# Kernel optimization log

Hardware: AMD Instinct MI355X
Metric: run time of the kernel (lower is better)

The kernel has to match this reference:

```python
import jax, jax.numpy as jnp
import numpy as np

N_ITER = 5
NMF_EPS = 1e-20
IP_EPS = 1e-20

M, J, I, K = 2, 2000, 2049, 8  # channels == sources, frames, freq bins, NMF bases


def setup_inputs() -> dict:
    key = jax.random.key(0)
    k1, k2, k3 = jax.random.split(key, 3)
    X = jax.random.normal(k1, (M, J, I, 2), dtype=jnp.float32)
    lo = 1e-08
    T0 = jax.random.uniform(k2, (I, K, M), dtype=jnp.float32) * (1 - lo) + lo
    V0 = jax.random.uniform(k3, (K, J, M), dtype=jnp.float32) * (1 - lo) + lo
    return {"X": X, "T0": T0, "V0": V0}


def nmf_update(T, V, Y, eps):
    # T: (I,K), V: (K,J), Y: (I,J) complex
    P = jnp.abs(Y) ** 2                       # power spectrogram (I,J)
    R = T @ V                                  # low-rank model (I,J)
    T = T * jnp.sqrt(((P / (R * R)) @ V.T) / ((1.0 / R) @ V.T))
    T = jnp.maximum(T, eps)
    R = T @ V
    V = V * jnp.sqrt((T.T @ (P / (R * R))) / (T.T @ (1.0 / R)))
    V = jnp.maximum(V, eps)
    R = T @ V
    return T, V, R


def reference(X, T0, V0):
    Mc, Jc, Ic, _ = X.shape
    N = Mc
    # view_as_complex(X.permute(2,0,1,3)) -> (I, M, J) complex
    Xc = jnp.transpose(X[..., 0] + 1j * X[..., 1], (2, 0, 1)).astype(jnp.complex64)
    eye_M = jnp.eye(Mc, dtype=jnp.complex64)
    W = jnp.broadcast_to(eye_M, (Ic, N, Mc))   # (I, N, M)
    T, V = T0, V0

    def body(carry, _):
        W, T, V = carry
        Y = jnp.einsum('inm,imj->inj', W, Xc)  # (I, N, J)
        for n in range(N):
            Tn, Vn, Rn = nmf_update(T[:, :, n], V[:, :, n], Y[:, n, :], NMF_EPS)
            T = T.at[:, :, n].set(Tn)
            V = V.at[:, :, n].set(Vn)
            inv_Rn = 1.0 / (Rn + IP_EPS)                       # (I, J)
            Xw = Xc * jnp.sqrt(inv_Rn)[:, None, :]             # (I, M, J)
            D = jnp.einsum('imj,ikj->imk', Xw, jnp.conj(Xw)) / Jc  # (I, M, M)
            Dreg = D + IP_EPS * eye_M
            A = jnp.einsum('inm,imk->ink', W, Dreg)            # (I, M, M)
            e_n = jnp.broadcast_to(eye_M[:, n], (Ic, Mc))
            b = jnp.linalg.solve(A, e_n[..., None])[..., 0]    # (I, M)
            quad = jnp.einsum('im,imk,ik->i', jnp.conj(b), Dreg, b)
            denom = jnp.sqrt(jnp.real(quad) + IP_EPS)          # (I,)
            W = W.at[:, n, :].set(jnp.conj(b / denom[:, None]))
        return (W, T, V), None

    (W, T, V), _ = jax.lax.scan(body, (W, T, V), None, length=N_ITER)
    Y = jnp.einsum('inm,imj->inj', W, Xc)                      # (I, N, J)
    Yp = jnp.transpose(Y, (1, 2, 0))                           # (N, J, I)
    return jnp.stack([jnp.real(Yp), jnp.imag(Yp)], axis=-1)    # (N, J, I, 2)
```

## Files before the change

### kernel.cpp

```cpp
#include <hip/hip_runtime.h>
#include <hip/hip_bf16.h>

#define M_CH 2
#define J_F 2000
#define I_F 2049
#define K_B 8
#define N_IT 5
#define NMF_EPS 1e-20f
#define IP_EPS 1e-20f

__global__ void k_init(const float* __restrict__ T0, const float* __restrict__ V0,
                       float* __restrict__ T, float* __restrict__ V, float* __restrict__ W) {
  int t = blockIdx.x * blockDim.x + threadIdx.x;
  int stride = gridDim.x * blockDim.x;
  for (int idx = t; idx < 2 * I_F * K_B; idx += stride) {
    int n = idx / (I_F * K_B);
    int r = idx % (I_F * K_B);
    int i = r / K_B, k = r % K_B;
    T[idx] = T0[(i * K_B + k) * M_CH + n];
  }
  for (int idx = t; idx < 2 * K_B * J_F; idx += stride) {
    int n = idx / (K_B * J_F);
    int r = idx % (K_B * J_F);
    int k = r / J_F, j = r % J_F;
    V[idx] = V0[(k * J_F + j) * M_CH + n];
  }
  for (int i = t; i < I_F; i += stride) {
    W[i * 8 + 0] = 1.f; W[i * 8 + 1] = 0.f; W[i * 8 + 2] = 0.f; W[i * 8 + 3] = 0.f;
    W[i * 8 + 4] = 0.f; W[i * 8 + 5] = 0.f; W[i * 8 + 6] = 1.f; W[i * 8 + 7] = 0.f;
  }
}

__global__ __launch_bounds__(256) void k_pack(const float2* __restrict__ X,
                                              float4* __restrict__ Xp) {
  const int i = blockIdx.x * 256 + threadIdx.x;
  if (i >= I_F) return;
  const int j0 = blockIdx.y * 8;
  const int jend = min(8, J_F - j0);
  for (int jj = 0; jj < jend; ++jj) {
    const int j = j0 + jj;
    float2 a = X[(size_t)j * I_F + i];
    float2 b = X[(size_t)(J_F + j) * I_F + i];
    Xp[(size_t)j * I_F + i] = make_float4(a.x, a.y, b.x, b.y);
  }
}

__global__ __launch_bounds__(256) void k_packT(const float2* __restrict__ X,
                                               float4* __restrict__ Xpt) {
  __shared__ float4 Tl[32][33];
  const int tid = threadIdx.x;
  const int i0 = blockIdx.x * 32, j0 = blockIdx.y * 32;
  const int la = tid & 31, su = tid >> 5;
#pragma unroll
  for (int p = 0; p < 4; ++p) {
    int jj = su + p * 8;
    int i = i0 + la, j = j0 + jj;
    if (i < I_F && j < J_F) {
      float2 a = X[(size_t)j * I_F + i];
      float2 b = X[(size_t)(J_F + j) * I_F + i];
      Tl[la][jj] = make_float4(a.x, a.y, b.x, b.y);
    }
  }
  __syncthreads();
#pragma unroll
  for (int p = 0; p < 4; ++p) {
    int ii = su + p * 8;
    int i = i0 + ii, j = j0 + la;
    if (i < I_F && j < J_F) Xpt[(size_t)i * J_F + j] = Tl[ii][la];
  }
}

__device__ __forceinline__ float4 load_x(const float4* Xp, const float2* X,
                                         int pk, size_t j, int i) {
  if (pk) return Xp[j * I_F + i];
  float2 a = X[j * I_F + i];
  float2 b = X[(size_t)J_F * I_F + j * I_F + i];
  return make_float4(a.x, a.y, b.x, b.y);
}

__device__ __forceinline__ float4 load_xt(const float4* Xpt, const float2* X,
                                          int pk, int i, int j) {
  if (pk) return Xpt[(size_t)i * J_F + j];
  float2 a = X[(size_t)j * I_F + i];
  float2 b = X[(size_t)(J_F + j) * I_F + i];
  return make_float4(a.x, a.y, b.x, b.y);
}

template<int PK>
__global__ __launch_bounds__(256) void k_T_rows(const float4* __restrict__ Xpt,
                                                const float2* __restrict__ X,
                                                const float* __restrict__ W,
                                                float* __restrict__ T,
                                                const float* __restrict__ V) {
  const int i = blockIdx.x;
  const int tid = threadIdx.x;
  float tr0[K_B], tr1[K_B];
#pragma unroll
  for (int k = 0; k < K_B; ++k) {
    tr0[k] = T[(size_t)i * 8 + k];
    tr1[k] = T[((size_t)I_F + i) * 8 + k];
  }
  const float4 w0 = ((const float4*)W)[i * 2];
  const float4 w1 = ((const float4*)W)[i * 2 + 1];
  float num0[K_B] = {}, den0[K_B] = {}, num1[K_B] = {}, den1[K_B] = {};
  for (int j = tid; j < J_F; j += 256) {
    float4 x = load_xt(Xpt, X, PK, i, j);
    float yr = w0.x * x.x - w0.y * x.y + w0.z * x.z - w0.w * x.w;
    float yi = w0.x * x.y + w0.y * x.x + w0.z * x.w + w0.w * x.z;
    float p0 = yr * yr + yi * yi;
    float zr = w1.x * x.x - w1.y * x.y + w1.z * x.z - w1.w * x.w;
    float zi = w1.x * x.y + w1.y * x.x + w1.z * x.w + w1.w * x.z;
    float p1 = zr * zr + zi * zi;
    float v0[K_B], v1[K_B];
    float R0 = 0.f, R1 = 0.f;
#pragma unroll
    for (int k = 0; k < K_B; ++k) {
      v0[k] = V[(size_t)k * J_F + j];           R0 += tr0[k] * v0[k];
      v1[k] = V[(size_t)(K_B + k) * J_F + j];   R1 += tr1[k] * v1[k];
    }
    float a0 = p0 / (R0 * R0), b0 = 1.0f / R0;
    float a1 = p1 / (R1 * R1), b1 = 1.0f / R1;
#pragma unroll
    for (int k = 0; k < K_B; ++k) {
      num0[k] += a0 * v0[k]; den0[k] += b0 * v0[k];
      num1[k] += a1 * v1[k]; den1[k] += b1 * v1[k];
    }
  }
  __shared__ float red[4][32];
  const int lane = tid & 63, wid = tid >> 6;
#pragma unroll
  for (int k = 0; k < K_B; ++k) {
    float a0 = num0[k], b0 = den0[k], a1 = num1[k], b1 = den1[k];
#pragma unroll
    for (int off = 32; off > 0; off >>= 1) {
      a0 += __shfl_xor(a0, off, 64);
      b0 += __shfl_xor(b0, off, 64);
      a1 += __shfl_xor(a1, off, 64);
      b1 += __shfl_xor(b1, off, 64);
    }
    if (lane == 0) {
      red[wid][k] = a0; red[wid][8 + k] = b0;
      red[wid][16 + k] = a1; red[wid][24 + k] = b1;
    }
  }
  __syncthreads();
  if (tid < 32) red[0][tid] = red[0][tid] + red[1][tid] + red[2][tid] + red[3][tid];
  __syncthreads();
  if (tid < 16) {
    int n = tid >> 3, k = tid & 7;
    float nu = red[0][n * 16 + k];
    float de = red[0][n * 16 + 8 + k];
    size_t idx = ((size_t)n * I_F + i) * 8 + k;
    float told = T[idx];
    T[idx] = fmaxf(told * sqrtf(nu / de), NMF_EPS);
  }
}

template<int PK>
__global__ __launch_bounds__(256) void k_v_update(const float4* __restrict__ Xp,
                                                  const float2* __restrict__ X,
                                                  const float* __restrict__ W,
                                                  const float* __restrict__ T,
                                                  float* __restrict__ V) {
  const int j = blockIdx.x;
  const int tid = threadIdx.x;
  float vold0[K_B], vold1[K_B];
#pragma unroll
  for (int k = 0; k < K_B; ++k) {
    vold0[k] = V[(size_t)k * J_F + j];
    vold1[k] = V[(size_t)(K_B + k) * J_F + j];
  }
  float num0[K_B] = {}, den0[K_B] = {}, num1[K_B] = {}, den1[K_B] = {};
  const float* T1 = T + (size_t)I_F * K_B;
  for (int i = tid; i < I_F; i += 256) {
    float4 x = load_x(Xp, X, PK, (size_t)j, i);
    const float4 wa = ((const float4*)W)[i * 2];
    const float4 wb = ((const float4*)W)[i * 2 + 1];
    float yr = wa.x * x.x - wa.y * x.y + wa.z * x.z - wa.w * x.w;
    float yi = wa.x * x.y + wa.y * x.x + wa.z * x.w + wa.w * x.z;
    float p0 = yr * yr + yi * yi;
    float zr = wb.x * x.x - wb.y * x.y + wb.z * x.z - wb.w * x.w;
    float zi = wb.x * x.y + wb.y * x.x + wb.z * x.w + wb.w * x.z;
    float p1 = zr * zr + zi * zi;
    const float4 ta = *(const float4*)&T[i * 8];
    const float4 tb = *(const float4*)&T[i * 8 + 4];
    const float4 tc = *(const float4*)&T1[i * 8];
    const float4 td = *(const float4*)&T1[i * 8 + 4];
    float t0[K_B] = {ta.x, ta.y, ta.z, ta.w, tb.x, tb.y, tb.z, tb.w};
    float t1[K_B] = {tc.x, tc.y, tc.z, tc.w, td.x, td.y, td.z, td.w};
    float R0 = 0.f, R1 = 0.f;
#pragma unroll
    for (int k = 0; k < K_B; ++k) { R0 += t0[k] * vold0[k]; R1 += t1[k] * vold1[k]; }
    float a0 = p0 / (R0 * R0), b0 = 1.0f / R0;
    float a1 = p1 / (R1 * R1), b1 = 1.0f / R1;
#pragma unroll
    for (int k = 0; k < K_B; ++k) {
      num0[k] += a0 * t0[k]; den0[k] += b0 * t0[k];
      num1[k] += a1 * t1[k]; den1[k] += b1 * t1[k];
    }
  }
  __shared__ float red[4][32];
  const int lane = tid & 63, wid = tid >> 6;
#pragma unroll
  for (int k = 0; k < K_B; ++k) {
    float a0 = num0[k], b0 = den0[k], a1 = num1[k], b1 = den1[k];
#pragma unroll
    for (int off = 32; off > 0; off >>= 1) {
      a0 += __shfl_xor(a0, off, 64);
      b0 += __shfl_xor(b0, off, 64);
      a1 += __shfl_xor(a1, off, 64);
      b1 += __shfl_xor(b1, off, 64);
    }
    if (lane == 0) {
      red[wid][k] = a0; red[wid][8 + k] = b0;
      red[wid][16 + k] = a1; red[wid][24 + k] = b1;
    }
  }
  __syncthreads();
  if (tid < 32) red[0][tid] = red[0][tid] + red[1][tid] + red[2][tid] + red[3][tid];
  __syncthreads();
  if (tid < 16) {
    int n = tid >> 3, k = tid & 7;
    float nu = red[0][n * 16 + k];
    float de = red[0][n * 16 + 8 + k];
    size_t idx = ((size_t)n * K_B + k) * J_F + j;
    float vo = V[idx];
    V[idx] = fmaxf(vo * sqrtf(nu / de), NMF_EPS);
  }
}

template<int PK>
__global__ __launch_bounds__(256) void k_d_rows(const float4* __restrict__ Xpt,
                                                const float2* __restrict__ X,
                                                const float* __restrict__ T,
                                                const float* __restrict__ V,
                                                float* __restrict__ W) {
  const int i = blockIdx.x;
  const int tid = threadIdx.x;
  float tr0[K_B], tr1[K_B];
#pragma unroll
  for (int k = 0; k < K_B; ++k) {
    tr0[k] = T[(size_t)i * K_B + k];
    tr1[k] = T[((size_t)I_F + i) * K_B + k];
  }
  float acc[8] = {};
  for (int j = tid; j < J_F; j += 256) {
    float4 x = load_xt(Xpt, X, PK, i, j);
    float R0 = 0.f, R1 = 0.f;
#pragma unroll
    for (int k = 0; k < K_B; ++k) {
      R0 += tr0[k] * V[(size_t)k * J_F + j];
      R1 += tr1[k] * V[(size_t)(K_B + k) * J_F + j];
    }
    float wv0 = 1.0f / (R0 + IP_EPS);
    float wv1 = 1.0f / (R1 + IP_EPS);
    float p00 = x.x * x.x + x.y * x.y;
    float p11 = x.z * x.z + x.w * x.w;
    float pr = x.x * x.z + x.y * x.w;
    float pi = x.y * x.z - x.x * x.w;
    acc[0] += wv0 * p00; acc[1] += wv0 * p11; acc[2] += wv0 * pr; acc[3] += wv0 * pi;
    acc[4] += wv1 * p00; acc[5] += wv1 * p11; acc[6] += wv1 * pr; acc[7] += wv1 * pi;
  }
  __shared__ float red[4][8];
  const int lane = tid & 63, wid = tid >> 6;
#pragma unroll
  for (int v = 0; v < 8; ++v) {
    float a = acc[v];
#pragma unroll
    for (int off = 32; off > 0; off >>= 1) a += __shfl_xor(a, off, 64);
    if (lane == 0) red[wid][v] = a;
  }
  __syncthreads();
  if (tid < 8) red[0][tid] = red[0][tid] + red[1][tid] + red[2][tid] + red[3][tid];
  __syncthreads();
  if (tid == 0) {
    float4 wa = ((const float4*)W)[i * 2];
    float4 wb = ((const float4*)W)[i * 2 + 1];
    float w00r = wa.x, w00i = wa.y, w01r = wa.z, w01i = wa.w;
    float w10r = wb.x, w10i = wb.y, w11r = wb.z, w11i = wb.w;
    const float invJ = 1.0f / (float)J_F;
#pragma unroll
    for (int n = 0; n < 2; ++n) {
      float d00 = red[0][n * 4 + 0] * invJ + IP_EPS;
      float d11 = red[0][n * 4 + 1] * invJ + IP_EPS;
      float d01r = red[0][n * 4 + 2] * invJ;
      float d01i = red[0][n * 4 + 3] * invJ;
      float A00r = w00r * d00 + (w01r * d01r + w01i * d01i);
      float A00i = w00i * d00 + (w01i * d01r - w01r * d01i);
      float A01r = (w00r * d01r - w00i * d01i) + w01r * d11;
      float A01i = (w00r * d01i + w00i * d01r) + w01i * d11;
      float A10r = w10r * d00 + (w11r * d01r + w11i * d01i);
      float A10i = w10i * d00 + (w11i * d01r - w11r * d01i);
      float A11r = (w10r * d01r - w10i * d01i) + w11r * d11;
      float A11i = (w10r * d01i + w10i * d01r) + w11i * d11;
      float detr = (A00r * A11r - A00i * A11i) - (A01r * A10r - A01i * A10i);
      float deti = (A00r * A11i + A00i * A11r) - (A01r * A10i + A01i * A10r);
      float idet = 1.0f / (detr * detr + deti * deti);
      float n0r, n0i, n1r, n1i;
      if (n == 0) { n0r = A11r; n0i = A11i; n1r = -A10r; n1i = -A10i; }
      else        { n0r = -A01r; n0i = -A01i; n1r = A00r; n1i = A00i; }
      float b0r = (n0r * detr + n0i * deti) * idet;
      float b0i = (n0i * detr - n0r * deti) * idet;
      float b1r = (n1r * detr + n1i * deti) * idet;
      float b1i = (n1i * detr - n1r * deti) * idet;
      float cr = d01r * b1r - d01i * b1i;
      float ci = d01r * b1i + d01i * b1r;
      float quad = d00 * (b0r * b0r + b0i * b0i) + d11 * (b1r * b1r + b1i * b1i)
                 + 2.0f * (b0r * cr + b0i * ci);
      float s = 1.0f / sqrtf(quad + IP_EPS);
      if (n == 0) { w00r = b0r * s; w00i = -b0i * s; w01r = b1r * s; w01i = -b1i * s; }
      else        { w10r = b0r * s; w10i = -b0i * s; w11r = b1r * s; w11i = -b1i * s; }
    }
    ((float4*)W)[i * 2]     = make_float4(w00r, w00i, w01r, w01i);
    ((float4*)W)[i * 2 + 1] = make_float4(w10r, w10i, w11r, w11i);
  }
}

template<int PK>
__global__ __launch_bounds__(256) void k_final(const float4* __restrict__ Xp,
                                               const float2* __restrict__ X,
                                               const float* __restrict__ W,
                                               float2* __restrict__ out) {
  const int i = blockIdx.x * 256 + threadIdx.x;
  if (i >= I_F) return;
  const float4 wa = ((const float4*)W)[i * 2];
  const float4 wb = ((const float4*)W)[i * 2 + 1];
  const int j0 = blockIdx.y * 8;
  const int jend = min(8, J_F - j0);
  for (int jj = 0; jj < jend; ++jj) {
    const int j = j0 + jj;
    float4 x = load_x(Xp, X, PK, (size_t)j, i);
    float y0r = wa.x * x.x - wa.y * x.y + wa.z * x.z - wa.w * x.w;
    float y0i = wa.x * x.y + wa.y * x.x + wa.z * x.w + wa.w * x.z;
    out[(size_t)j * I_F + i] = make_float2(y0r, y0i);
    float y1r = wb.x * x.x - wb.y * x.y + wb.z * x.z - wb.w * x.w;
    float y1i = wb.x * x.y + wb.y * x.x + wb.z * x.w + wb.w * x.z;
    out[(size_t)(J_F + j) * I_F + i] = make_float2(y1r, y1i);
  }
}

extern "C" void kernel_launch(void* const* d_in, const int* in_sizes, int n_in,
                              void* d_out, int out_size, void* d_ws, size_t ws_size,
                              hipStream_t stream) {
  const float2* X = (const float2*)d_in[0];
  const float* T0 = (const float*)d_in[1];
  const float* V0 = (const float*)d_in[2];
  char* ws = (char*)d_ws;
  size_t off = 0;
  auto alloc = [&](size_t bytes) -> void* {
    void* p = ws + off;
    off = (off + bytes + 255) & ~(size_t)255;
    return p;
  };
  float* W = (float*)alloc((size_t)I_F * 8 * 4);
  float* T = (float*)alloc((size_t)2 * I_F * K_B * 4);
  float* V = (float*)alloc((size_t)2 * K_B * J_F * 4);
  const size_t x_sz = (size_t)J_F * I_F * 16;
  float4* Xpt = nullptr;
  float4* Xp = nullptr;
  if (off + x_sz <= ws_size) Xpt = (float4*)alloc(x_sz);
  if (Xpt && off + x_sz <= ws_size) Xp = (float4*)alloc(x_sz);
  const int pkt = Xpt != nullptr, pkj = Xp != nullptr;

  k_init<<<128, 256, 0, stream>>>(T0, V0, T, V, W);
  if (pkt) k_packT<<<dim3(65, 63), 256, 0, stream>>>(X, Xpt);
  if (pkj) k_pack<<<dim3(9, 250), 256, 0, stream>>>(X, Xp);

  if (pkt && pkj) {
    for (int it = 0; it < N_IT; ++it) {
      k_T_rows<1><<<I_F, 256, 0, stream>>>(Xpt, X, W, T, V);
      k_v_update<1><<<J_F, 256, 0, stream>>>(Xp, X, W, T, V);
      k_d_rows<1><<<I_F, 256, 0, stream>>>(Xpt, X, T, V, W);
    }
    k_final<1><<<dim3(9, 250), 256, 0, stream>>>(Xp, X, W, (float2*)d_out);
  } else if (pkt) {
    for (int it = 0; it < N_IT; ++it) {
      k_T_rows<1><<<I_F, 256, 0, stream>>>(Xpt, X, W, T, V);
      k_v_update<0><<<J_F, 256, 0, stream>>>(nullptr, X, W, T, V);
      k_d_rows<1><<<I_F, 256, 0, stream>>>(Xpt, X, T, V, W);
    }
    k_final<0><<<dim3(9, 250), 256, 0, stream>>>(nullptr, X, W, (float2*)d_out);
  } else {
    for (int it = 0; it < N_IT; ++it) {
      k_T_rows<0><<<I_F, 256, 0, stream>>>(nullptr, X, W, T, V);
      k_v_update<0><<<J_F, 256, 0, stream>>>(nullptr, X, W, T, V);
      k_d_rows<0><<<I_F, 256, 0, stream>>>(nullptr, X, T, V, W);
    }
    k_final<0><<<dim3(9, 250), 256, 0, stream>>>(nullptr, X, W, (float2*)d_out);
  }
}
```

Measured before the change: 490.2 us.

## Fuse D/W update with next-iteration T update and interleave T/V per row

```diff
diff --git a/kernel.cpp b/kernel.cpp
--- a/kernel.cpp
+++ b/kernel.cpp
@@ -1,5 +1,4 @@
 #include <hip/hip_runtime.h>
-#include <hip/hip_bf16.h>
 
 #define M_CH 2
 #define J_F 2000
@@ -9,66 +8,9 @@
 #define NMF_EPS 1e-20f
 #define IP_EPS 1e-20f
 
-__global__ void k_init(const float* __restrict__ T0, const float* __restrict__ V0,
-                       float* __restrict__ T, float* __restrict__ V, float* __restrict__ W) {
-  int t = blockIdx.x * blockDim.x + threadIdx.x;
-  int stride = gridDim.x * blockDim.x;
-  for (int idx = t; idx < 2 * I_F * K_B; idx += stride) {
-    int n = idx / (I_F * K_B);
-    int r = idx % (I_F * K_B);
-    int i = r / K_B, k = r % K_B;
-    T[idx] = T0[(i * K_B + k) * M_CH + n];
-  }
-  for (int idx = t; idx < 2 * K_B * J_F; idx += stride) {
-    int n = idx / (K_B * J_F);
-    int r = idx % (K_B * J_F);
-    int k = r / J_F, j = r % J_F;
-    V[idx] = V0[(k * J_F + j) * M_CH + n];
-  }
-  for (int i = t; i < I_F; i += stride) {
-    W[i * 8 + 0] = 1.f; W[i * 8 + 1] = 0.f; W[i * 8 + 2] = 0.f; W[i * 8 + 3] = 0.f;
-    W[i * 8 + 4] = 0.f; W[i * 8 + 5] = 0.f; W[i * 8 + 6] = 1.f; W[i * 8 + 7] = 0.f;
-  }
-}
-
-__global__ __launch_bounds__(256) void k_pack(const float2* __restrict__ X,
-                                              float4* __restrict__ Xp) {
-  const int i = blockIdx.x * 256 + threadIdx.x;
-  if (i >= I_F) return;
-  const int j0 = blockIdx.y * 8;
-  const int jend = min(8, J_F - j0);
-  for (int jj = 0; jj < jend; ++jj) {
-    const int j = j0 + jj;
-    float2 a = X[(size_t)j * I_F + i];
-    float2 b = X[(size_t)(J_F + j) * I_F + i];
-    Xp[(size_t)j * I_F + i] = make_float4(a.x, a.y, b.x, b.y);
-  }
-}
-
-__global__ __launch_bounds__(256) void k_packT(const float2* __restrict__ X,
-                                               float4* __restrict__ Xpt) {
-  __shared__ float4 Tl[32][33];
-  const int tid = threadIdx.x;
-  const int i0 = blockIdx.x * 32, j0 = blockIdx.y * 32;
-  const int la = tid & 31, su = tid >> 5;
-#pragma unroll
-  for (int p = 0; p < 4; ++p) {
-    int jj = su + p * 8;
-    int i = i0 + la, j = j0 + jj;
-    if (i < I_F && j < J_F) {
-      float2 a = X[(size_t)j * I_F + i];
-      float2 b = X[(size_t)(J_F + j) * I_F + i];
-      Tl[la][jj] = make_float4(a.x, a.y, b.x, b.y);
-    }
-  }
-  __syncthreads();
-#pragma unroll
-  for (int p = 0; p < 4; ++p) {
-    int ii = su + p * 8;
-    int i = i0 + ii, j = j0 + la;
-    if (i < I_F && j < J_F) Xpt[(size_t)i * J_F + j] = Tl[ii][la];
-  }
-}
+#define NB_PACKT (65 * 63)
+#define NB_PACK (9 * 250)
+#define NB_INIT 128
 
 __device__ __forceinline__ float4 load_x(const float4* Xp, const float2* X,
                                          int pk, size_t j, int i) {
@@ -86,38 +28,101 @@
   return make_float4(a.x, a.y, b.x, b.y);
 }
 
-template<int PK>
-__global__ __launch_bounds__(256) void k_T_rows(const float4* __restrict__ Xpt,
-                                                const float2* __restrict__ X,
-                                                const float* __restrict__ W,
-                                                float* __restrict__ T,
-                                                const float* __restrict__ V) {
-  const int i = blockIdx.x;
+template<int PKT, int PKJ>
+__global__ __launch_bounds__(256) void k_setup(const float2* __restrict__ X,
+                                               const float* __restrict__ T0,
+                                               const float* __restrict__ V0,
+                                               float* __restrict__ Tt,
+                                               float* __restrict__ Vt,
+                                               float* __restrict__ W,
+                                               float4* __restrict__ Xpt,
+                                               float4* __restrict__ Xp) {
+  int b = blockIdx.x;
   const int tid = threadIdx.x;
-  float tr0[K_B], tr1[K_B];
-#pragma unroll
-  for (int k = 0; k < K_B; ++k) {
-    tr0[k] = T[(size_t)i * 8 + k];
-    tr1[k] = T[((size_t)I_F + i) * 8 + k];
-  }
-  const float4 w0 = ((const float4*)W)[i * 2];
-  const float4 w1 = ((const float4*)W)[i * 2 + 1];
+  if (b < NB_PACKT) {
+    if (!PKT) return;
+    __shared__ float4 Tl[32][33];
+    const int i0 = (b % 65) * 32, j0 = (b / 65) * 32;
+    const int la = tid & 31, su = tid >> 5;
+#pragma unroll
+    for (int p = 0; p < 4; ++p) {
+      int jj = su + p * 8;
+      int i = i0 + la, j = j0 + jj;
+      if (i < I_F && j < J_F) {
+        float2 a = X[(size_t)j * I_F + i];
+        float2 c = X[(size_t)(J_F + j) * I_F + i];
+        Tl[la][jj] = make_float4(a.x, a.y, c.x, c.y);
+      }
+    }
+    __syncthreads();
+#pragma unroll
+    for (int p = 0; p < 4; ++p) {
+      int ii = su + p * 8;
+      int i = i0 + ii, j = j0 + la;
+      if (i < I_F && j < J_F) Xpt[(size_t)i * J_F + j] = Tl[ii][la];
+    }
+    return;
+  }
+  b -= NB_PACKT;
+  if (b < NB_PACK) {
+    if (!PKJ) return;
+    const int i = (b % 9) * 256 + tid;
+    if (i >= I_F) return;
+    const int j0 = (b / 9) * 8;
+    const int jend = min(8, J_F - j0);
+    for (int jj = 0; jj < jend; ++jj) {
+      const int j = j0 + jj;
+      float2 a = X[(size_t)j * I_F + i];
+      float2 c = X[(size_t)(J_F + j) * I_F + i];
+      Xp[(size_t)j * I_F + i] = make_float4(a.x, a.y, c.x, c.y);
+    }
+    return;
+  }
+  b -= NB_PACK;
+  int t = b * 256 + tid;
+  const int stride = NB_INIT * 256;
+  for (int idx = t; idx < I_F * 16; idx += stride) {
+    int i = idx >> 4, c = idx & 15;
+    int n = c >> 3, k = c & 7;
+    Tt[idx] = T0[(i * K_B + k) * M_CH + n];
+  }
+  for (int idx = t; idx < J_F * 16; idx += stride) {
+    int j = idx >> 4, c = idx & 15;
+    int n = c >> 3, k = c & 7;
+    Vt[idx] = V0[(k * J_F + j) * M_CH + n];
+  }
+  for (int i = t; i < I_F; i += stride) {
+    W[i * 8 + 0] = 1.f; W[i * 8 + 1] = 0.f; W[i * 8 + 2] = 0.f; W[i * 8 + 3] = 0.f;
+    W[i * 8 + 4] = 0.f; W[i * 8 + 5] = 0.f; W[i * 8 + 6] = 1.f; W[i * 8 + 7] = 0.f;
+  }
+}
+
+__device__ __forceinline__ void t_body(const int i, const float4* __restrict__ Xpt,
+                                       const float2* __restrict__ X, const int pkt,
+                                       const float4 w0, const float4 w1,
+                                       float* __restrict__ Tt, const float* __restrict__ Vt,
+                                       float (*red)[32]) {
+  const int tid = threadIdx.x;
+  const float4* tt = (const float4*)(Tt + (size_t)i * 16);
+  const float4 ta = tt[0], tb = tt[1], tc = tt[2], td = tt[3];
+  const float tr0[K_B] = {ta.x, ta.y, ta.z, ta.w, tb.x, tb.y, tb.z, tb.w};
+  const float tr1[K_B] = {tc.x, tc.y, tc.z, tc.w, td.x, td.y, td.z, td.w};
   float num0[K_B] = {}, den0[K_B] = {}, num1[K_B] = {}, den1[K_B] = {};
   for (int j = tid; j < J_F; j += 256) {
-    float4 x = load_xt(Xpt, X, PK, i, j);
+    float4 x = load_xt(Xpt, X, pkt, i, j);
     float yr = w0.x * x.x - w0.y * x.y + w0.z * x.z - w0.w * x.w;
     float yi = w0.x * x.y + w0.y * x.x + w0.z * x.w + w0.w * x.z;
     float p0 = yr * yr + yi * yi;
     float zr = w1.x * x.x - w1.y * x.y + w1.z * x.z - w1.w * x.w;
     float zi = w1.x * x.y + w1.y * x.x + w1.z * x.w + w1.w * x.z;
     float p1 = zr * zr + zi * zi;
-    float v0[K_B], v1[K_B];
+    const float4* vv = (const float4*)(Vt + (size_t)j * 16);
+    const float4 va = vv[0], vb = vv[1], vc = vv[2], vd = vv[3];
+    const float v0[K_B] = {va.x, va.y, va.z, va.w, vb.x, vb.y, vb.z, vb.w};
+    const float v1[K_B] = {vc.x, vc.y, vc.z, vc.w, vd.x, vd.y, vd.z, vd.w};
     float R0 = 0.f, R1 = 0.f;
 #pragma unroll
-    for (int k = 0; k < K_B; ++k) {
-      v0[k] = V[(size_t)k * J_F + j];           R0 += tr0[k] * v0[k];
-      v1[k] = V[(size_t)(K_B + k) * J_F + j];   R1 += tr1[k] * v1[k];
-    }
+    for (int k = 0; k < K_B; ++k) { R0 += tr0[k] * v0[k]; R1 += tr1[k] * v1[k]; }
     float a0 = p0 / (R0 * R0), b0 = 1.0f / R0;
     float a1 = p1 / (R1 * R1), b1 = 1.0f / R1;
 #pragma unroll
@@ -126,7 +131,6 @@
       num1[k] += a1 * v1[k]; den1[k] += b1 * v1[k];
     }
   }
-  __shared__ float red[4][32];
   const int lane = tid & 63, wid = tid >> 6;
 #pragma unroll
   for (int k = 0; k < K_B; ++k) {
@@ -150,30 +154,25 @@
     int n = tid >> 3, k = tid & 7;
     float nu = red[0][n * 16 + k];
     float de = red[0][n * 16 + 8 + k];
-    size_t idx = ((size_t)n * I_F + i) * 8 + k;
-    float told = T[idx];
-    T[idx] = fmaxf(told * sqrtf(nu / de), NMF_EPS);
-  }
-}
-
-template<int PK>
-__global__ __launch_bounds__(256) void k_v_update(const float4* __restrict__ Xp,
-                                                  const float2* __restrict__ X,
-                                                  const float* __restrict__ W,
-                                                  const float* __restrict__ T,
-                                                  float* __restrict__ V) {
-  const int j = blockIdx.x;
+    float told = Tt[(size_t)i * 16 + tid];
+    Tt[(size_t)i * 16 + tid] = fmaxf(told * sqrtf(nu / de), NMF_EPS);
+  }
+  __syncthreads();
+}
+
+__device__ __forceinline__ void v_body(const int j, const float4* __restrict__ Xp,
+                                       const float2* __restrict__ X, const int pkj,
+                                       const float* __restrict__ W,
+                                       const float* __restrict__ Tt,
+                                       float* __restrict__ Vt, float (*red)[32]) {
   const int tid = threadIdx.x;
-  float vold0[K_B], vold1[K_B];
-#pragma unroll
-  for (int k = 0; k < K_B; ++k) {
-    vold0[k] = V[(size_t)k * J_F + j];
-    vold1[k] = V[(size_t)(K_B + k) * J_F + j];
-  }
+  const float4* vv = (const float4*)(Vt + (size_t)j * 16);
+  const float4 va = vv[0], vb = vv[1], vc = vv[2], vd = vv[3];
+  const float vold0[K_B] = {va.x, va.y, va.z, va.w, vb.x, vb.y, vb.z, vb.w};
+  const float vold1[K_B] = {vc.x, vc.y, vc.z, vc.w, vd.x, vd.y, vd.z, vd.w};
   float num0[K_B] = {}, den0[K_B] = {}, num1[K_B] = {}, den1[K_B] = {};
-  const float* T1 = T + (size_t)I_F * K_B;
   for (int i = tid; i < I_F; i += 256) {
-    float4 x = load_x(Xp, X, PK, (size_t)j, i);
+    float4 x = load_x(Xp, X, pkj, (size_t)j, i);
     const float4 wa = ((const float4*)W)[i * 2];
     const float4 wb = ((const float4*)W)[i * 2 + 1];
     float yr = wa.x * x.x - wa.y * x.y + wa.z * x.z - wa.w * x.w;
@@ -182,12 +181,10 @@
     float zr = wb.x * x.x - wb.y * x.y + wb.z * x.z - wb.w * x.w;
     float zi = wb.x * x.y + wb.y * x.x + wb.z * x.w + wb.w * x.z;
     float p1 = zr * zr + zi * zi;
-    const float4 ta = *(const float4*)&T[i * 8];
-    const float4 tb = *(const float4*)&T[i * 8 + 4];
-    const float4 tc = *(const float4*)&T1[i * 8];
-    const float4 td = *(const float4*)&T1[i * 8 + 4];
-    float t0[K_B] = {ta.x, ta.y, ta.z, ta.w, tb.x, tb.y, tb.z, tb.w};
-    float t1[K_B] = {tc.x, tc.y, tc.z, tc.w, td.x, td.y, td.z, td.w};
+    const float4* tt = (const float4*)(Tt + (size_t)i * 16);
+    const float4 ta = tt[0], tb = tt[1], tc = tt[2], td = tt[3];
+    const float t0[K_B] = {ta.x, ta.y, ta.z, ta.w, tb.x, tb.y, tb.z, tb.w};
+    const float t1[K_B] = {tc.x, tc.y, tc.z, tc.w, td.x, td.y, td.z, td.w};
     float R0 = 0.f, R1 = 0.f;
 #pragma unroll
     for (int k = 0; k < K_B; ++k) { R0 += t0[k] * vold0[k]; R1 += t1[k] * vold1[k]; }
@@ -199,7 +196,6 @@
       num1[k] += a1 * t1[k]; den1[k] += b1 * t1[k];
     }
   }
-  __shared__ float red[4][32];
   const int lane = tid & 63, wid = tid >> 6;
 #pragma unroll
   for (int k = 0; k < K_B; ++k) {
@@ -223,35 +219,33 @@
     int n = tid >> 3, k = tid & 7;
     float nu = red[0][n * 16 + k];
     float de = red[0][n * 16 + 8 + k];
-    size_t idx = ((size_t)n * K_B + k) * J_F + j;
-    float vo = V[idx];
-    V[idx] = fmaxf(vo * sqrtf(nu / de), NMF_EPS);
-  }
-}
-
-template<int PK>
-__global__ __launch_bounds__(256) void k_d_rows(const float4* __restrict__ Xpt,
-                                                const float2* __restrict__ X,
-                                                const float* __restrict__ T,
-                                                const float* __restrict__ V,
-                                                float* __restrict__ W) {
-  const int i = blockIdx.x;
+    float vo = Vt[(size_t)j * 16 + tid];
+    Vt[(size_t)j * 16 + tid] = fmaxf(vo * sqrtf(nu / de), NMF_EPS);
+  }
+  __syncthreads();
+}
+
+__device__ __forceinline__ void d_body(const int i, const float4* __restrict__ Xpt,
+                                       const float2* __restrict__ X, const int pkt,
+                                       const float* __restrict__ Tt,
+                                       const float* __restrict__ Vt,
+                                       float* __restrict__ W, float (*red)[32],
+                                       float* wrow) {
   const int tid = threadIdx.x;
-  float tr0[K_B], tr1[K_B];
-#pragma unroll
-  for (int k = 0; k < K_B; ++k) {
-    tr0[k] = T[(size_t)i * K_B + k];
-    tr1[k] = T[((size_t)I_F + i) * K_B + k];
-  }
+  const float4* tt = (const float4*)(Tt + (size_t)i * 16);
+  const float4 ta = tt[0], tb = tt[1], tc = tt[2], td = tt[3];
+  const float tr0[K_B] = {ta.x, ta.y, ta.z, ta.w, tb.x, tb.y, tb.z, tb.w};
+  const float tr1[K_B] = {tc.x, tc.y, tc.z, tc.w, td.x, td.y, td.z, td.w};
   float acc[8] = {};
   for (int j = tid; j < J_F; j += 256) {
-    float4 x = load_xt(Xpt, X, PK, i, j);
+    float4 x = load_xt(Xpt, X, pkt, i, j);
+    const float4* vv = (const float4*)(Vt + (size_t)j * 16);
+    const float4 va = vv[0], vb = vv[1], vc = vv[2], vd = vv[3];
+    const float v0[K_B] = {va.x, va.y, va.z, va.w, vb.x, vb.y, vb.z, vb.w};
+    const float v1[K_B] = {vc.x, vc.y, vc.z, vc.w, vd.x, vd.y, vd.z, vd.w};
     float R0 = 0.f, R1 = 0.f;
 #pragma unroll
-    for (int k = 0; k < K_B; ++k) {
-      R0 += tr0[k] * V[(size_t)k * J_F + j];
-      R1 += tr1[k] * V[(size_t)(K_B + k) * J_F + j];
-    }
+    for (int k = 0; k < K_B; ++k) { R0 += tr0[k] * v0[k]; R1 += tr1[k] * v1[k]; }
     float wv0 = 1.0f / (R0 + IP_EPS);
     float wv1 = 1.0f / (R1 + IP_EPS);
     float p00 = x.x * x.x + x.y * x.y;
@@ -261,7 +255,6 @@
     acc[0] += wv0 * p00; acc[1] += wv0 * p11; acc[2] += wv0 * pr; acc[3] += wv0 * pi;
     acc[4] += wv1 * p00; acc[5] += wv1 * p11; acc[6] += wv1 * pr; acc[7] += wv1 * pi;
   }
-  __shared__ float red[4][8];
   const int lane = tid & 63, wid = tid >> 6;
 #pragma unroll
   for (int v = 0; v < 8; ++v) {
@@ -313,6 +306,49 @@
     }
     ((float4*)W)[i * 2]     = make_float4(w00r, w00i, w01r, w01i);
     ((float4*)W)[i * 2 + 1] = make_float4(w10r, w10i, w11r, w11i);
+    wrow[0] = w00r; wrow[1] = w00i; wrow[2] = w01r; wrow[3] = w01i;
+    wrow[4] = w10r; wrow[5] = w10i; wrow[6] = w11r; wrow[7] = w11i;
+  }
+  __syncthreads();
+}
+
+template<int PK>
+__global__ __launch_bounds__(256) void k_T(const float4* __restrict__ Xpt,
+                                           const float2* __restrict__ X,
+                                           const float* __restrict__ W,
+                                           float* __restrict__ Tt,
+                                           const float* __restrict__ Vt) {
+  __shared__ float red[4][32];
+  const int i = blockIdx.x;
+  const float4 w0 = ((const float4*)W)[i * 2];
+  const float4 w1 = ((const float4*)W)[i * 2 + 1];
+  t_body(i, Xpt, X, PK, w0, w1, Tt, Vt, red);
+}
+
+template<int PK>
+__global__ __launch_bounds__(256) void k_V(const float4* __restrict__ Xp,
+                                           const float2* __restrict__ X,
+                                           const float* __restrict__ W,
+                                           const float* __restrict__ Tt,
+                                           float* __restrict__ Vt) {
+  __shared__ float red[4][32];
+  v_body(blockIdx.x, Xp, X, PK, W, Tt, Vt, red);
+}
+
+template<int PK, int LAST>
+__global__ __launch_bounds__(256) void k_DT(const float4* __restrict__ Xpt,
+                                            const float2* __restrict__ X,
+                                            float* __restrict__ Tt,
+                                            const float* __restrict__ Vt,
+                                            float* __restrict__ W) {
+  __shared__ float red[4][32];
+  __shared__ float wrow[8];
+  const int i = blockIdx.x;
+  d_body(i, Xpt, X, PK, Tt, Vt, W, red, wrow);
+  if (!LAST) {
+    const float4 w0 = make_float4(wrow[0], wrow[1], wrow[2], wrow[3]);
+    const float4 w1 = make_float4(wrow[4], wrow[5], wrow[6], wrow[7]);
+    t_body(i, Xpt, X, PK, w0, w1, Tt, Vt, red);
   }
 }
 
@@ -345,6 +381,7 @@
   const float2* X = (const float2*)d_in[0];
   const float* T0 = (const float*)d_in[1];
   const float* V0 = (const float*)d_in[2];
+  float2* outp = (float2*)d_out;
   char* ws = (char*)d_ws;
   size_t off = 0;
   auto alloc = [&](size_t bytes) -> void* {
@@ -353,39 +390,47 @@
     return p;
   };
   float* W = (float*)alloc((size_t)I_F * 8 * 4);
-  float* T = (float*)alloc((size_t)2 * I_F * K_B * 4);
-  float* V = (float*)alloc((size_t)2 * K_B * J_F * 4);
+  float* Tt = (float*)alloc((size_t)I_F * 16 * 4);
+  float* Vt = (float*)alloc((size_t)J_F * 16 * 4);
   const size_t x_sz = (size_t)J_F * I_F * 16;
   float4* Xpt = nullptr;
   float4* Xp = nullptr;
   if (off + x_sz <= ws_size) Xpt = (float4*)alloc(x_sz);
   if (Xpt && off + x_sz <= ws_size) Xp = (float4*)alloc(x_sz);
-  const int pkt = Xpt != nullptr, pkj = Xp != nullptr;
-
-  k_init<<<128, 256, 0, stream>>>(T0, V0, T, V, W);
-  if (pkt) k_packT<<<dim3(65, 63), 256, 0, stream>>>(X, Xpt);
-  if (pkj) k_pack<<<dim3(9, 250), 256, 0, stream>>>(X, Xp);
-
-  if (pkt && pkj) {
+  const int NB_SETUP = NB_PACKT + NB_PACK + NB_INIT;
+
+  if (Xpt && Xp) {
+    k_setup<1, 1><<<NB_SETUP, 256, 0, stream>>>(X, T0, V0, Tt, Vt, W, Xpt, Xp);
+    k_T<1><<<I_F, 256, 0, stream>>>(Xpt, X, W, Tt, Vt);
     for (int it = 0; it < N_IT; ++it) {
-      k_T_rows<1><<<I_F, 256, 0, stream>>>(Xpt, X, W, T, V);
-      k_v_update<1><<<J_F, 256, 0, stream>>>(Xp, X, W, T, V);
-      k_d_rows<1><<<I_F, 256, 0, stream>>>(Xpt, X, T, V, W);
-    }
-    k_final<1><<<dim3(9, 250), 256, 0, stream>>>(Xp, X, W, (float2*)d_out);
-  } else if (pkt) {
+      k_V<1><<<J_F, 256, 0, stream>>>(Xp, X, W, Tt, Vt);
+      if (it < N_IT - 1)
+        k_DT<1, 0><<<I_F, 256, 0, stream>>>(Xpt, X, Tt, Vt, W);
+      else
+        k_DT<1, 1><<<I_F, 256, 0, stream>>>(Xpt, X, Tt, Vt, W);
+    }
+    k_final<1><<<dim3(9, 250), 256, 0, stream>>>(Xp, X, W, outp);
+  } else if (Xpt) {
+    k_setup<1, 0><<<NB_SETUP, 256, 0, stream>>>(X, T0, V0, Tt, Vt, W, Xpt, nullptr);
+    k_T<1><<<I_F, 256, 0, stream>>>(Xpt, X, W, Tt, Vt);
     for (int it = 0; it < N_IT; ++it) {
-      k_T_rows<1><<<I_F, 256, 0, stream>>>(Xpt, X, W, T, V);
-      k_v_update<0><<<J_F, 256, 0, stream>>>(nullptr, X, W, T, V);
-      k_d_rows<1><<<I_F, 256, 0, stream>>>(Xpt, X, T, V, W);
-    }
-    k_final<0><<<dim3(9, 250), 256, 0, stream>>>(nullptr, X, W, (float2*)d_out);
+      k_V<0><<<J_F, 256, 0, stream>>>(nullptr, X, W, Tt, Vt);
+      if (it < N_IT - 1)
+        k_DT<1, 0><<<I_F, 256, 0, stream>>>(Xpt, X, Tt, Vt, W);
+      else
+        k_DT<1, 1><<<I_F, 256, 0, stream>>>(Xpt, X, Tt, Vt, W);
+    }
+    k_final<0><<<dim3(9, 250), 256, 0, stream>>>(nullptr, X, W, outp);
   } else {
+    k_setup<0, 0><<<NB_SETUP, 256, 0, stream>>>(X, T0, V0, Tt, Vt, W, nullptr, nullptr);
+    k_T<0><<<I_F, 256, 0, stream>>>(nullptr, X, W, Tt, Vt);
     for (int it = 0; it < N_IT; ++it) {
-      k_T_rows<0><<<I_F, 256, 0, stream>>>(nullptr, X, W, T, V);
-      k_v_update<0><<<J_F, 256, 0, stream>>>(nullptr, X, W, T, V);
-      k_d_rows<0><<<I_F, 256, 0, stream>>>(nullptr, X, T, V, W);
-    }
-    k_final<0><<<dim3(9, 250), 256, 0, stream>>>(nullptr, X, W, (float2*)d_out);
-  }
-}
+      k_V<0><<<J_F, 256, 0, stream>>>(nullptr, X, W, Tt, Vt);
+      if (it < N_IT - 1)
+        k_DT<0, 0><<<I_F, 256, 0, stream>>>(nullptr, X, Tt, Vt, W);
+      else
+        k_DT<0, 1><<<I_F, 256, 0, stream>>>(nullptr, X, Tt, Vt, W);
+    }
+    k_final<0><<<dim3(9, 250), 256, 0, stream>>>(nullptr, X, W, outp);
+  }
+}
```

After: 586.2 us. +19.6%, slower.
